# Kernel tuning notes

Hardware: AMD Instinct MI355X
Metric: run time of the kernel (lower is better)

The kernel has to match this reference:

```python
import jax, jax.numpy as jnp
import numpy as np

B, N, DIN, D, HID, C, K = 16, 1024, 768, 512, 128, 20, 64
H = W = 32
EPS = 1e-5  # BatchNorm eps (inference mode with running stats)


def _conv(x, w, pad=0, dil=1):
    return jax.lax.conv_general_dilated(
        x, w, (1, 1), [(pad, pad), (pad, pad)],
        rhs_dilation=(dil, dil),
        dimension_numbers=('NCHW', 'OIHW', 'NCHW'))


def _bn(x, g, b, m, v):
    inv = jax.lax.rsqrt(v + EPS)
    return (x - m[None, :, None, None]) * (g * inv)[None, :, None, None] + b[None, :, None, None]


def _l2norm(x):
    n = jnp.sqrt(jnp.sum(x * x, axis=-1, keepdims=True))
    return x / jnp.maximum(n, 1e-12)  # matches F.normalize(eps=1e-12)


def setup_inputs():
    key = jax.random.key(0)
    ks = jax.random.split(key, 12)

    def conv_w(k, o, i, kh, kw):
        return jax.random.normal(k, (o, i, kh, kw), jnp.float32) / np.sqrt(i * kh * kw)

    def bn_p(k, c):
        k1, k2 = jax.random.split(k)
        return (jnp.ones(c, jnp.float32), jnp.zeros(c, jnp.float32),
                0.1 * jax.random.normal(k1, (c,), jnp.float32),
                jax.random.uniform(k2, (c,), jnp.float32, 0.5, 1.5))

    g0, b0, m0, v0 = bn_p(ks[3], D)
    gr, br, mr, vr = bn_p(ks[4], HID)
    gl, bl, ml, vl = bn_p(ks[5], HID)
    gg, bg, mg, vg = bn_p(ks[6], HID)
    gp, bp, mp, vp = bn_p(ks[7], D)
    return {
        'patch_feats': jax.random.normal(ks[0], (B, N, DIN), jnp.float32),
        'protos': _l2norm(jax.random.normal(ks[1], (C, K, D), jnp.float32)),  # hybrid protos, L2-normed as in __init__
        'w0': conv_w(ks[2], D, DIN, 1, 1), 'g0': g0, 'b0': b0, 'm0': m0, 'v0': v0,
        'wr': conv_w(ks[8], HID, D, 1, 1), 'gr': gr, 'br': br, 'mr': mr, 'vr': vr,
        'wl': conv_w(ks[9], HID, HID, 3, 3), 'gl': gl, 'bl': bl, 'ml': ml, 'vl': vl,
        'wg': conv_w(ks[10], HID, HID, 3, 3), 'gg': gg, 'bg': bg, 'mg': mg, 'vg': vg,
        'wp': conv_w(ks[11], D, 2 * HID, 1, 1), 'gp': gp, 'bp': bp, 'mp': mp, 'vp': vp,
        'wf': conv_w(jax.random.fold_in(key, 99), D, D, 1, 1),
        'bf': jnp.zeros(D, jnp.float32),
        'logit_scale': jnp.float32(10.0),
    }


def reference(patch_feats, protos, w0, g0, b0, m0, v0, wr, gr, br, mr, vr,
              wl, gl, bl, ml, vl, wg, gg, bg, mg, vg, wp, gp, bp, mp, vp,
              wf, bf, logit_scale):
    Bq, Nq, Din = patch_feats.shape
    x = patch_feats.transpose(0, 2, 1).reshape(Bq, Din, H, W)
    # adapter: 1x1 conv -> BN -> ReLU
    x = jax.nn.relu(_bn(_conv(x, w0), g0, b0, m0, v0))
    # ResidualContextBlock
    res = x
    o = jax.nn.relu(_bn(_conv(x, wr), gr, br, mr, vr))
    l = jax.nn.relu(_bn(_conv(o, wl, pad=1), gl, bl, ml, vl))
    g = jax.nn.relu(_bn(_conv(o, wg, pad=2, dil=2), gg, bg, mg, vg))
    o = _bn(_conv(jnp.concatenate([l, g], axis=1), wp), gp, bp, mp, vp)
    x = jax.nn.relu(o + res)
    # final 1x1 conv (with bias)
    x = _conv(x, wf) + bf[None, :, None, None]
    # back to [B, N, D], L2 normalize
    x = x.reshape(Bq, D, Nq).transpose(0, 2, 1)
    x = _l2norm(x)
    # per-class cosine sims + double max reduction (vectorized over classes)
    sims = jnp.einsum('bnd,ckd->bcnk', x, protos)  # [B,C,N,K]
    A = sims.max(axis=-1)                          # [B,C,N] patch->proto max
    act_maps = A.reshape(Bq, C, H, W)
    logits = A.max(axis=-1) * logit_scale          # [B,C]
    return logits, act_maps, x
```

## Files before the change

kernel.cpp:

```cpp
#include <hip/hip_runtime.h>
#include <math.h>

#define BN_EPS 1e-5f

typedef __attribute__((ext_vector_type(8))) short short8v;
typedef __attribute__((ext_vector_type(8))) unsigned short ushort8v;
typedef __attribute__((ext_vector_type(4))) float f32x4;

__device__ __forceinline__ unsigned short f2b(float f) {
    unsigned int u = __float_as_uint(f);
    return (unsigned short)((u + 0x7FFFu + ((u >> 16) & 1u)) >> 16);
}
__device__ __forceinline__ float b2f(unsigned short h) {
    return __uint_as_float(((unsigned int)h) << 16);
}

typedef __attribute__((address_space(1))) const unsigned int gas_uint;
typedef __attribute__((address_space(3))) unsigned int las_uint;
__device__ __forceinline__ void gload16(const void* g, void* l) {
    __builtin_amdgcn_global_load_lds((gas_uint*)g, (las_uint*)l, 16, 0, 0);
}

__global__ __launch_bounds__(256) void f2b_kernel(
    const float* __restrict__ in, unsigned short* __restrict__ out, int n8)
{
    int i = blockIdx.x * 256 + threadIdx.x;
    if (i >= n8) return;
    const float4* p = (const float4*)(in + (size_t)i * 8);
    float4 a = p[0], b = p[1];
    ushort8v r;
    r[0] = f2b(a.x); r[1] = f2b(a.y); r[2] = f2b(a.z); r[3] = f2b(a.w);
    r[4] = f2b(b.x); r[5] = f2b(b.y); r[6] = f2b(b.z); r[7] = f2b(b.w);
    *(ushort8v*)(out + (size_t)i * 8) = r;
}

__global__ __launch_bounds__(256) void f2b_multi(
    const float* __restrict__ w0, const float* __restrict__ wr,
    const float* __restrict__ wp, const float* __restrict__ wf,
    const float* __restrict__ prot,
    unsigned short* __restrict__ w0o, unsigned short* __restrict__ wro,
    unsigned short* __restrict__ wpo, unsigned short* __restrict__ wfo,
    unsigned short* __restrict__ proto)
{
    int i = blockIdx.x * 256 + threadIdx.x;
    const float* src; unsigned short* dst; int off;
    if      (i <  49152) { src = w0;   dst = w0o;   off = i; }
    else if (i <  57344) { src = wr;   dst = wro;   off = i - 49152; }
    else if (i <  73728) { src = wp;   dst = wpo;   off = i - 57344; }
    else if (i < 106496) { src = wf;   dst = wfo;   off = i - 73728; }
    else if (i < 188416) { src = prot; dst = proto; off = i - 106496; }
    else return;
    const float4* p = (const float4*)(src + (size_t)off * 8);
    float4 a = p[0], b = p[1];
    ushort8v r;
    r[0] = f2b(a.x); r[1] = f2b(a.y); r[2] = f2b(a.z); r[3] = f2b(a.w);
    r[4] = f2b(b.x); r[5] = f2b(b.y); r[6] = f2b(b.z); r[7] = f2b(b.w);
    *(ushort8v*)(dst + (size_t)off * 8) = r;
}

__global__ __launch_bounds__(256) void convw_kernel(
    const float* __restrict__ wl, const float* __restrict__ wg,
    unsigned short* __restrict__ out)
{
    int i = blockIdx.x * 256 + threadIdx.x;
    if (i >= 294912) return;
    int br = i >= 147456;
    int j  = i - br * 147456;
    int tap = j >> 14, oc = (j >> 7) & 127, ic = j & 127;
    const float* src = br ? wg : wl;
    out[i] = f2b(src[((oc << 7) + ic) * 9 + tap]);
}

__global__ __launch_bounds__(256) void zero_kernel(unsigned short* __restrict__ p, int n8)
{
    int i = blockIdx.x * 256 + threadIdx.x;
    if (i >= n8) return;
    ushort8v z;
#pragma unroll
    for (int k = 0; k < 8; ++k) z[k] = 0;
    *(ushort8v*)(p + (size_t)i * 8) = z;
}

template <int EPI>
__global__ __launch_bounds__(256) void mfma_gemm(
    const unsigned short* __restrict__ A, int lda,
    const unsigned short* __restrict__ Wt, int ldw,
    void* __restrict__ outp, int ldc, int Kdim,
    const float* __restrict__ bng, const float* __restrict__ bnb,
    const float* __restrict__ bnm, const float* __restrict__ bnv,
    const unsigned short* __restrict__ res, int ldres,
    const float* __restrict__ bias)
{
    __shared__ short8v Asta[512];
    __shared__ short8v Bsta[512];
    const int t  = threadIdx.x;
    const int l  = t & 63, wv = t >> 6;
    const int wm = wv >> 1, wn = wv & 1;
    const int m0 = blockIdx.x << 7, n0 = blockIdx.y << 7;

    const int r0  = t & 127;
    const int kb0 = t >> 7;

    const unsigned short* Ap = A  + (size_t)(m0 + r0) * lda + kb0 * 8;
    const unsigned short* Bp = Wt + (size_t)(n0 + r0) * ldw + kb0 * 8;

    short8v* aD0 = Asta + wv * 64;
    short8v* aD1 = Asta + wv * 64 + 256;
    short8v* bD0 = Bsta + wv * 64;
    short8v* bD1 = Bsta + wv * 64 + 256;

    f32x4 acc[4][4];
#pragma unroll
    for (int mf = 0; mf < 4; ++mf)
#pragma unroll
        for (int nf = 0; nf < 4; ++nf)
#pragma unroll
            for (int j = 0; j < 4; ++j) acc[mf][nf][j] = 0.f;

    const int arow = wm * 64 + (l & 15);
    const int brow = wn * 64 + (l & 15);
    const int kq   = l >> 4;

    for (int k0 = 0; k0 < Kdim; k0 += 32) {
        __syncthreads();
        gload16(Ap + k0,      aD0);
        gload16(Ap + k0 + 16, aD1);
        gload16(Bp + k0,      bD0);
        gload16(Bp + k0 + 16, bD1);
        __syncthreads();
        short8v af[4], bfv[4];
#pragma unroll
        for (int mf = 0; mf < 4; ++mf) af[mf]  = Asta[kq * 128 + arow + mf * 16];
#pragma unroll
        for (int nf = 0; nf < 4; ++nf) bfv[nf] = Bsta[kq * 128 + brow + nf * 16];
#pragma unroll
        for (int mf = 0; mf < 4; ++mf)
#pragma unroll
            for (int nf = 0; nf < 4; ++nf)
                acc[mf][nf] = __builtin_amdgcn_mfma_f32_16x16x32_bf16(
                    af[mf], bfv[nf], acc[mf][nf], 0, 0, 0);
    }

    float s[4], sh[4];
    int cols[4];
#pragma unroll
    for (int nf = 0; nf < 4; ++nf) {
        int col = n0 + wn * 64 + nf * 16 + (l & 15);
        cols[nf] = col;
        if (EPI == 2) { s[nf] = 1.f; sh[nf] = bias[col]; }
        else {
            float sc = bng[col] * rsqrtf(bnv[col] + BN_EPS);
            s[nf]  = sc;
            sh[nf] = bnb[col] - bnm[col] * sc;
        }
    }
#pragma unroll
    for (int mf = 0; mf < 4; ++mf) {
#pragma unroll
        for (int j = 0; j < 4; ++j) {
            int row = m0 + wm * 64 + mf * 16 + kq * 4 + j;
#pragma unroll
            for (int nf = 0; nf < 4; ++nf) {
                float v = acc[mf][nf][j] * s[nf] + sh[nf];
                if (EPI == 1) v += b2f(res[(size_t)row * ldres + cols[nf]]);
                if (EPI != 2) v = fmaxf(v, 0.f);
                if (EPI == 2) {
                    ((float*)outp)[(size_t)row * ldc + cols[nf]] = v;
                } else if (EPI == 3) {
                    int b = row >> 10, h = (row >> 5) & 31, ww = row & 31;
                    size_t pidx = ((size_t)(b * 36 + h + 2) * 36 + (ww + 2)) * 128 + cols[nf];
                    ((unsigned short*)outp)[pidx] = f2b(v);
                } else {
                    ((unsigned short*)outp)[(size_t)row * ldc + cols[nf]] = f2b(v);
                }
            }
        }
    }
}

__global__ __launch_bounds__(256) void conv_mfma(
    const unsigned short* __restrict__ opad,
    const unsigned short* __restrict__ wt_all,
    const float* __restrict__ g1, const float* __restrict__ b1,
    const float* __restrict__ m1, const float* __restrict__ v1,
    const float* __restrict__ g2, const float* __restrict__ b2,
    const float* __restrict__ m2, const float* __restrict__ v2,
    unsigned short* __restrict__ lg)
{
    __shared__ short8v Asta[1024];
    __shared__ short8v Bsta[2048];
    const int t = threadIdx.x;
    const int l = t & 63, wv = t >> 6;
    const int wm = wv >> 1, wn = wv & 1;
    const int m0 = blockIdx.x << 6;
    const int br = blockIdx.y;
    const int dil = 1 + br;
    const unsigned short* wtb = wt_all + (size_t)br * 147456;

    const int r0  = t & 63,  kb0 = t >> 6;
    const int rb  = t & 127, kbb = t >> 7;
    const int m   = m0 + r0;
    const int bb  = m >> 10, h = (m >> 5) & 31, wc = m & 31;
    const ptrdiff_t pbase = ((ptrdiff_t)(bb * 36 + h + 2) * 36 + (wc + 2)) * 128;
    const unsigned short* ApT = opad + pbase + kb0 * 8;
    const unsigned short* BpT = wtb + (size_t)rb * 128 + kbb * 8;

    f32x4 acc[2][4];
#pragma unroll
    for (int mf = 0; mf < 2; ++mf)
#pragma unroll
        for (int nf = 0; nf < 4; ++nf)
#pragma unroll
            for (int j = 0; j < 4; ++j) acc[mf][nf][j] = 0.f;

    const int arow = wm * 32 + (l & 15);
    const int bcol = wn * 64 + (l & 15);
    const int kq   = l >> 4;

    for (int tap = 0; tap < 9; ++tap) {
        const int dh = tap / 3 - 1, dw = tap % 3 - 1;
        const unsigned short* Ap = ApT + (ptrdiff_t)((dh * 36 + dw) * dil) * 128;
        const unsigned short* Bp = BpT + (size_t)tap * 16384;
        __syncthreads();
#pragma unroll
        for (int i = 0; i < 4; ++i)
            gload16(Ap + 32 * i, Asta + wv * 64 + 256 * i);
#pragma unroll
        for (int i = 0; i < 8; ++i)
            gload16(Bp + 16 * i, Bsta + wv * 64 + 256 * i);
        __syncthreads();
#pragma unroll
        for (int kk = 0; kk < 4; ++kk) {
            short8v af[2], bfv[4];
            af[0] = Asta[(kq + 4 * kk) * 64 + arow];
            af[1] = Asta[(kq + 4 * kk) * 64 + arow + 16];
#pragma unroll
            for (int nf = 0; nf < 4; ++nf)
                bfv[nf] = Bsta[(kq + 4 * kk) * 128 + bcol + nf * 16];
#pragma unroll
            for (int mf = 0; mf < 2; ++mf)
#pragma unroll
                for (int nf = 0; nf < 4; ++nf)
                    acc[mf][nf] = __builtin_amdgcn_mfma_f32_16x16x32_bf16(
                        af[mf], bfv[nf], acc[mf][nf], 0, 0, 0);
        }
    }

    const float* gg = br ? g2 : g1;
    const float* gb = br ? b2 : b1;
    const float* gm = br ? m2 : m1;
    const float* gv = br ? v2 : v1;
    float s[4], sh[4];
    int cols[4];
#pragma unroll
    for (int nf = 0; nf < 4; ++nf) {
        int col = bcol + nf * 16;
        cols[nf] = col;
        float sc = gg[col] * rsqrtf(gv[col] + BN_EPS);
        s[nf]  = sc;
        sh[nf] = gb[col] - gm[col] * sc;
    }
#pragma unroll
    for (int mf = 0; mf < 2; ++mf) {
#pragma unroll
        for (int j = 0; j < 4; ++j) {
            int row = m0 + wm * 32 + mf * 16 + kq * 4 + j;
#pragma unroll
            for (int nf = 0; nf < 4; ++nf) {
                float v = fmaxf(acc[mf][nf][j] * s[nf] + sh[nf], 0.f);
                lg[(size_t)row * 256 + br * 128 + cols[nf]] = f2b(v);
            }
        }
    }
}

__global__ __launch_bounds__(256) void l2norm_rows(
    float* __restrict__ x, unsigned short* __restrict__ xn)
{
    const int t    = threadIdx.x;
    const int wv   = t >> 6, lane = t & 63;
    const int row  = (blockIdx.x << 2) + wv;
    float* p = x + (size_t)row * 512 + (lane << 3);
    float4 a = *(float4*)p;
    float4 b = *(float4*)(p + 4);
    float ss = a.x * a.x + a.y * a.y + a.z * a.z + a.w * a.w +
               b.x * b.x + b.y * b.y + b.z * b.z + b.w * b.w;
#pragma unroll
    for (int off = 32; off >= 1; off >>= 1) ss += __shfl_xor(ss, off);
    float sc = 1.f / fmaxf(sqrtf(ss), 1e-12f);
    a.x *= sc; a.y *= sc; a.z *= sc; a.w *= sc;
    b.x *= sc; b.y *= sc; b.z *= sc; b.w *= sc;
    *(float4*)p       = a;
    *(float4*)(p + 4) = b;
    ushort8v r;
    r[0] = f2b(a.x); r[1] = f2b(a.y); r[2] = f2b(a.z); r[3] = f2b(a.w);
    r[4] = f2b(b.x); r[5] = f2b(b.y); r[6] = f2b(b.z); r[7] = f2b(b.w);
    *(ushort8v*)(xn + (size_t)row * 512 + (lane << 3)) = r;
}

__global__ __launch_bounds__(256) void sims_mfma(
    const unsigned short* __restrict__ xn,
    const unsigned short* __restrict__ protos,
    float* __restrict__ act)
{
    __shared__ short8v Asta[512];
    __shared__ short8v Bsta[512];
    const int t = threadIdx.x;
    const int l = t & 63, wv = t >> 6;
    const int wm = wv >> 1, wn = wv & 1;
    const int m0 = blockIdx.x << 7;

    const int r0  = t & 127, kb0 = t >> 7;
    const unsigned short* Ap = xn + (size_t)(m0 + r0) * 512 + kb0 * 8;
    const unsigned short* Bp = protos + ((size_t)blockIdx.y * 128 + r0) * 512 + kb0 * 8;

    short8v* aD0 = Asta + wv * 64;
    short8v* aD1 = Asta + wv * 64 + 256;
    short8v* bD0 = Bsta + wv * 64;
    short8v* bD1 = Bsta + wv * 64 + 256;

    f32x4 acc[4][4];
#pragma unroll
    for (int mf = 0; mf < 4; ++mf)
#pragma unroll
        for (int nf = 0; nf < 4; ++nf)
#pragma unroll
            for (int j = 0; j < 4; ++j) acc[mf][nf][j] = 0.f;

    const int arow = wm * 64 + (l & 15);
    const int brow = wn * 64 + (l & 15);
    const int kq   = l >> 4;

    for (int k0 = 0; k0 < 512; k0 += 32) {
        __syncthreads();
        gload16(Ap + k0,      aD0);
        gload16(Ap + k0 + 16, aD1);
        gload16(Bp + k0,      bD0);
        gload16(Bp + k0 + 16, bD1);
        __syncthreads();
        short8v af[4], bfv[4];
#pragma unroll
        for (int mf = 0; mf < 4; ++mf) af[mf]  = Asta[kq * 128 + arow + mf * 16];
#pragma unroll
        for (int nf = 0; nf < 4; ++nf) bfv[nf] = Bsta[kq * 128 + brow + nf * 16];
#pragma unroll
        for (int mf = 0; mf < 4; ++mf)
#pragma unroll
            for (int nf = 0; nf < 4; ++nf)
                acc[mf][nf] = __builtin_amdgcn_mfma_f32_16x16x32_bf16(
                    af[mf], bfv[nf], acc[mf][nf], 0, 0, 0);
    }

    const int c = (blockIdx.y << 1) + wn;
#pragma unroll
    for (int mf = 0; mf < 4; ++mf) {
        float vj[4];
#pragma unroll
        for (int j = 0; j < 4; ++j) {
            float v = fmaxf(fmaxf(acc[mf][0][j], acc[mf][1][j]),
                            fmaxf(acc[mf][2][j], acc[mf][3][j]));
            v = fmaxf(v, __shfl_xor(v, 1));
            v = fmaxf(v, __shfl_xor(v, 2));
            v = fmaxf(v, __shfl_xor(v, 4));
            v = fmaxf(v, __shfl_xor(v, 8));
            vj[j] = v;
        }
        if ((l & 15) == 0) {
            int rowb = m0 + wm * 64 + mf * 16 + kq * 4;
#pragma unroll
            for (int j = 0; j < 4; ++j) {
                int row = rowb + j;
                int bb = row >> 10, n = row & 1023;
                act[(((size_t)(bb * 20 + c)) << 10) + n] = vj[j];
            }
        }
    }
}

__global__ __launch_bounds__(256) void logits_max(
    const float* __restrict__ act, const float* __restrict__ lsc,
    float* __restrict__ logits)
{
    const int bc = blockIdx.x;
    const int t  = threadIdx.x;
    float4 v = *(const float4*)(act + ((size_t)bc << 10) + (t << 2));
    float mx = fmaxf(fmaxf(v.x, v.y), fmaxf(v.z, v.w));
#pragma unroll
    for (int off = 32; off >= 1; off >>= 1) mx = fmaxf(mx, __shfl_xor(mx, off));
    __shared__ float wmred[4];
    if ((t & 63) == 0) wmred[t >> 6] = mx;
    __syncthreads();
    if (t == 0) {
        float m2 = fmaxf(fmaxf(wmred[0], wmred[1]), fmaxf(wmred[2], wmred[3]));
        logits[bc] = m2 * lsc[0];
    }
}

extern "C" void kernel_launch(void* const* d_in, const int* in_sizes, int n_in,
                              void* d_out, int out_size, void* d_ws, size_t ws_size,
                              hipStream_t stream)
{
    const float* pf   = (const float*)d_in[0];
    const float* prot = (const float*)d_in[1];
    const float* w0   = (const float*)d_in[2];
    const float* g0   = (const float*)d_in[3];
    const float* b0   = (const float*)d_in[4];
    const float* m0v  = (const float*)d_in[5];
    const float* v0   = (const float*)d_in[6];
    const float* wr   = (const float*)d_in[7];
    const float* gr   = (const float*)d_in[8];
    const float* br   = (const float*)d_in[9];
    const float* mr   = (const float*)d_in[10];
    const float* vr   = (const float*)d_in[11];
    const float* wl   = (const float*)d_in[12];
    const float* gl   = (const float*)d_in[13];
    const float* bl   = (const float*)d_in[14];
    const float* ml   = (const float*)d_in[15];
    const float* vl   = (const float*)d_in[16];
    const float* wg   = (const float*)d_in[17];
    const float* gG   = (const float*)d_in[18];
    const float* bG   = (const float*)d_in[19];
    const float* mG   = (const float*)d_in[20];
    const float* vG   = (const float*)d_in[21];
    const float* wp   = (const float*)d_in[22];
    const float* gp   = (const float*)d_in[23];
    const float* bp   = (const float*)d_in[24];
    const float* mp   = (const float*)d_in[25];
    const float* vp   = (const float*)d_in[26];
    const float* wf   = (const float*)d_in[27];
    const float* bf_  = (const float*)d_in[28];
    const float* lsc  = (const float*)d_in[29];

    char* ws = (char*)d_ws;
    unsigned short* pf_bf    = (unsigned short*)(ws);
    unsigned short* w0_bf    = (unsigned short*)(ws + 25165824);
    unsigned short* wr_bf    = (unsigned short*)(ws + 25952256);
    unsigned short* wt_bf    = (unsigned short*)(ws + 26083328);
    unsigned short* wp_bf    = (unsigned short*)(ws + 26673152);
    unsigned short* wf_bf    = (unsigned short*)(ws + 26935296);
    unsigned short* prot_bf  = (unsigned short*)(ws + 27459584);
    unsigned short* x1_bf    = (unsigned short*)(ws + 28770304);
    unsigned short* opad     = (unsigned short*)(ws + 45547520);
    unsigned short* lg_bf    = (unsigned short*)(ws + 50855936);
    unsigned short* x2_bf    = (unsigned short*)(ws + 59244544);
    unsigned short* xn_bf    = (unsigned short*)(ws + 76021760);

    float* out    = (float*)d_out;
    float* logits = out;
    float* act    = out + 320;
    float* xo     = out + 328000;

    f2b_kernel<<<6144, 256, 0, stream>>>(pf, pf_bf, 1572864);
    f2b_multi<<<736, 256, 0, stream>>>(w0, wr, wp, wf, prot,
                                       w0_bf, wr_bf, wp_bf, wf_bf, prot_bf);
    convw_kernel<<<1152, 256, 0, stream>>>(wl, wg, wt_bf);
    zero_kernel<<<1296, 256, 0, stream>>>(opad, 331776);

    mfma_gemm<0><<<dim3(128, 4), 256, 0, stream>>>(
        pf_bf, 768, w0_bf, 768, x1_bf, 512, 768,
        g0, b0, m0v, v0, nullptr, 0, nullptr);

    mfma_gemm<3><<<dim3(128, 1), 256, 0, stream>>>(
        x1_bf, 512, wr_bf, 512, opad, 0, 512,
        gr, br, mr, vr, nullptr, 0, nullptr);

    conv_mfma<<<dim3(256, 2), 256, 0, stream>>>(
        opad, wt_bf, gl, bl, ml, vl, gG, bG, mG, vG, lg_bf);

    mfma_gemm<1><<<dim3(128, 4), 256, 0, stream>>>(
        lg_bf, 256, wp_bf, 256, x2_bf, 512, 256,
        gp, bp, mp, vp, x1_bf, 512, nullptr);

    mfma_gemm<2><<<dim3(128, 4), 256, 0, stream>>>(
        x2_bf, 512, wf_bf, 512, xo, 512, 512,
        nullptr, nullptr, nullptr, nullptr, nullptr, 0, bf_);

    l2norm_rows<<<4096, 256, 0, stream>>>(xo, xn_bf);

    sims_mfma<<<dim3(128, 10), 256, 0, stream>>>(xn_bf, prot_bf, act);

    logits_max<<<320, 256, 0, stream>>>(act, lsc, logits);
}
```

Baseline: 202.0 us.

## Double-buffer LDS staging in GEMM, conv and sims kernels to overlap loads

Converts the three MFMA kernels from a single-buffered load/sync/compute loop to a double-buffered scheme. The next K-slice is prefetched into the alternate LDS buffer while the current slice's MFMAs run, and one barrier per iteration replaces two. The conv kernel now splits each tap into two 64-wide K halves so its per-stage LDS footprint fits the two buffers. Launch bounds with min 3 blocks per CU are also added, which may constrain register allocation.

After: 198.0 us. -2.0%, faster.

```diff
diff --git a/kernel.cpp b/kernel.cpp
--- a/kernel.cpp
+++ b/kernel.cpp
@@ -82,7 +82,7 @@
 }
 
 template <int EPI>
-__global__ __launch_bounds__(256) void mfma_gemm(
+__global__ __launch_bounds__(256, 3) void mfma_gemm(
     const unsigned short* __restrict__ A, int lda,
     const unsigned short* __restrict__ Wt, int ldw,
     void* __restrict__ outp, int ldc, int Kdim,
@@ -91,8 +91,8 @@
     const unsigned short* __restrict__ res, int ldres,
     const float* __restrict__ bias)
 {
-    __shared__ short8v Asta[512];
-    __shared__ short8v Bsta[512];
+    __shared__ short8v Asta[2][512];
+    __shared__ short8v Bsta[2][512];
     const int t  = threadIdx.x;
     const int l  = t & 63, wv = t >> 6;
     const int wm = wv >> 1, wn = wv & 1;
@@ -104,11 +104,6 @@
     const unsigned short* Ap = A  + (size_t)(m0 + r0) * lda + kb0 * 8;
     const unsigned short* Bp = Wt + (size_t)(n0 + r0) * ldw + kb0 * 8;
 
-    short8v* aD0 = Asta + wv * 64;
-    short8v* aD1 = Asta + wv * 64 + 256;
-    short8v* bD0 = Bsta + wv * 64;
-    short8v* bD1 = Bsta + wv * 64 + 256;
-
     f32x4 acc[4][4];
 #pragma unroll
     for (int mf = 0; mf < 4; ++mf)
@@ -121,25 +116,36 @@
     const int brow = wn * 64 + (l & 15);
     const int kq   = l >> 4;
 
-    for (int k0 = 0; k0 < Kdim; k0 += 32) {
-        __syncthreads();
-        gload16(Ap + k0,      aD0);
-        gload16(Ap + k0 + 16, aD1);
-        gload16(Bp + k0,      bD0);
-        gload16(Bp + k0 + 16, bD1);
-        __syncthreads();
+    const int nK = Kdim >> 5;
+
+#define STAGE_G(buf, k0)                                     \
+    do {                                                     \
+        gload16(Ap + (k0),      &Asta[buf][wv * 64]);        \
+        gload16(Ap + (k0) + 16, &Asta[buf][wv * 64 + 256]);  \
+        gload16(Bp + (k0),      &Bsta[buf][wv * 64]);        \
+        gload16(Bp + (k0) + 16, &Bsta[buf][wv * 64 + 256]);  \
+    } while (0)
+
+    STAGE_G(0, 0);
+    __syncthreads();
+    int cur = 0;
+    for (int ks = 0; ks < nK; ++ks) {
         short8v af[4], bfv[4];
 #pragma unroll
-        for (int mf = 0; mf < 4; ++mf) af[mf]  = Asta[kq * 128 + arow + mf * 16];
-#pragma unroll
-        for (int nf = 0; nf < 4; ++nf) bfv[nf] = Bsta[kq * 128 + brow + nf * 16];
+        for (int mf = 0; mf < 4; ++mf) af[mf]  = Asta[cur][kq * 128 + arow + mf * 16];
+#pragma unroll
+        for (int nf = 0; nf < 4; ++nf) bfv[nf] = Bsta[cur][kq * 128 + brow + nf * 16];
+        if (ks + 1 < nK) STAGE_G(cur ^ 1, (ks + 1) << 5);
 #pragma unroll
         for (int mf = 0; mf < 4; ++mf)
 #pragma unroll
             for (int nf = 0; nf < 4; ++nf)
                 acc[mf][nf] = __builtin_amdgcn_mfma_f32_16x16x32_bf16(
                     af[mf], bfv[nf], acc[mf][nf], 0, 0, 0);
-    }
+        __syncthreads();
+        cur ^= 1;
+    }
+#undef STAGE_G
 
     float s[4], sh[4];
     int cols[4];
@@ -178,7 +184,7 @@
     }
 }
 
-__global__ __launch_bounds__(256) void conv_mfma(
+__global__ __launch_bounds__(256, 3) void conv_mfma(
     const unsigned short* __restrict__ opad,
     const unsigned short* __restrict__ wt_all,
     const float* __restrict__ g1, const float* __restrict__ b1,
@@ -187,8 +193,8 @@
     const float* __restrict__ m2, const float* __restrict__ v2,
     unsigned short* __restrict__ lg)
 {
-    __shared__ short8v Asta[1024];
-    __shared__ short8v Bsta[2048];
+    __shared__ short8v Asta[2][512];
+    __shared__ short8v Bsta[2][1024];
     const int t = threadIdx.x;
     const int l = t & 63, wv = t >> 6;
     const int wm = wv >> 1, wn = wv & 1;
@@ -197,13 +203,12 @@
     const int dil = 1 + br;
     const unsigned short* wtb = wt_all + (size_t)br * 147456;
 
-    const int r0  = t & 63,  kb0 = t >> 6;
-    const int rb  = t & 127, kbb = t >> 7;
-    const int m   = m0 + r0;
-    const int bb  = m >> 10, h = (m >> 5) & 31, wc = m & 31;
+    const int r0 = t & 63;
+    const int m  = m0 + r0;
+    const int bb = m >> 10, h = (m >> 5) & 31, wc = m & 31;
     const ptrdiff_t pbase = ((ptrdiff_t)(bb * 36 + h + 2) * 36 + (wc + 2)) * 128;
-    const unsigned short* ApT = opad + pbase + kb0 * 8;
-    const unsigned short* BpT = wtb + (size_t)rb * 128 + kbb * 8;
+    const unsigned short* ApT = opad + pbase + (t >> 6) * 8;
+    const unsigned short* BpT = wtb + (size_t)(t & 127) * 128 + (t >> 7) * 8;
 
     f32x4 acc[2][4];
 #pragma unroll
@@ -217,47 +222,60 @@
     const int bcol = wn * 64 + (l & 15);
     const int kq   = l >> 4;
 
-    for (int tap = 0; tap < 9; ++tap) {
-        const int dh = tap / 3 - 1, dw = tap % 3 - 1;
-        const unsigned short* Ap = ApT + (ptrdiff_t)((dh * 36 + dw) * dil) * 128;
-        const unsigned short* Bp = BpT + (size_t)tap * 16384;
-        __syncthreads();
-#pragma unroll
-        for (int i = 0; i < 4; ++i)
-            gload16(Ap + 32 * i, Asta + wv * 64 + 256 * i);
-#pragma unroll
-        for (int i = 0; i < 8; ++i)
-            gload16(Bp + 16 * i, Bsta + wv * 64 + 256 * i);
-        __syncthreads();
-#pragma unroll
-        for (int kk = 0; kk < 4; ++kk) {
-            short8v af[2], bfv[4];
-            af[0] = Asta[(kq + 4 * kk) * 64 + arow];
-            af[1] = Asta[(kq + 4 * kk) * 64 + arow + 16];
+#define STAGE_C(buf, s)                                                        \
+    do {                                                                       \
+        int tap_ = (s) >> 1, hh_ = ((s) & 1) * 64;                             \
+        int dh_ = tap_ / 3 - 1, dw_ = tap_ % 3 - 1;                            \
+        const unsigned short* Ap_ = ApT + (ptrdiff_t)((dh_ * 36 + dw_) * dil) * 128 + hh_; \
+        const unsigned short* Bp_ = BpT + (size_t)tap_ * 16384 + hh_;          \
+        gload16(Ap_,      &Asta[buf][wv * 64]);                                \
+        gload16(Ap_ + 32, &Asta[buf][wv * 64 + 256]);                          \
+        gload16(Bp_,      &Bsta[buf][wv * 64]);                                \
+        gload16(Bp_ + 16, &Bsta[buf][wv * 64 + 256]);                          \
+        gload16(Bp_ + 32, &Bsta[buf][wv * 64 + 512]);                          \
+        gload16(Bp_ + 48, &Bsta[buf][wv * 64 + 768]);                          \
+    } while (0)
+
+    STAGE_C(0, 0);
+    __syncthreads();
+    int cur = 0;
+    for (int s = 0; s < 18; ++s) {
+        short8v af[2][2], bfv[2][4];
+#pragma unroll
+        for (int kk = 0; kk < 2; ++kk) {
+            int kb = kk * 4 + kq;
+            af[kk][0] = Asta[cur][kb * 64 + arow];
+            af[kk][1] = Asta[cur][kb * 64 + arow + 16];
 #pragma unroll
             for (int nf = 0; nf < 4; ++nf)
-                bfv[nf] = Bsta[(kq + 4 * kk) * 128 + bcol + nf * 16];
+                bfv[kk][nf] = Bsta[cur][kb * 128 + bcol + nf * 16];
+        }
+        if (s + 1 < 18) STAGE_C(cur ^ 1, s + 1);
+#pragma unroll
+        for (int kk = 0; kk < 2; ++kk)
 #pragma unroll
             for (int mf = 0; mf < 2; ++mf)
 #pragma unroll
                 for (int nf = 0; nf < 4; ++nf)
                     acc[mf][nf] = __builtin_amdgcn_mfma_f32_16x16x32_bf16(
-                        af[mf], bfv[nf], acc[mf][nf], 0, 0, 0);
-        }
-    }
+                        af[kk][mf], bfv[kk][nf], acc[mf][nf], 0, 0, 0);
+        __syncthreads();
+        cur ^= 1;
+    }
+#undef STAGE_C
 
     const float* gg = br ? g2 : g1;
     const float* gb = br ? b2 : b1;
     const float* gm = br ? m2 : m1;
     const float* gv = br ? v2 : v1;
-    float s[4], sh[4];
+    float s4[4], sh[4];
     int cols[4];
 #pragma unroll
     for (int nf = 0; nf < 4; ++nf) {
         int col = bcol + nf * 16;
         cols[nf] = col;
         float sc = gg[col] * rsqrtf(gv[col] + BN_EPS);
-        s[nf]  = sc;
+        s4[nf] = sc;
         sh[nf] = gb[col] - gm[col] * sc;
     }
 #pragma unroll
@@ -267,7 +285,7 @@
             int row = m0 + wm * 32 + mf * 16 + kq * 4 + j;
 #pragma unroll
             for (int nf = 0; nf < 4; ++nf) {
-                float v = fmaxf(acc[mf][nf][j] * s[nf] + sh[nf], 0.f);
+                float v = fmaxf(acc[mf][nf][j] * s4[nf] + sh[nf], 0.f);
                 lg[(size_t)row * 256 + br * 128 + cols[nf]] = f2b(v);
             }
         }
@@ -298,13 +316,13 @@
     *(ushort8v*)(xn + (size_t)row * 512 + (lane << 3)) = r;
 }
 
-__global__ __launch_bounds__(256) void sims_mfma(
+__global__ __launch_bounds__(256, 3) void sims_mfma(
     const unsigned short* __restrict__ xn,
     const unsigned short* __restrict__ protos,
     float* __restrict__ act)
 {
-    __shared__ short8v Asta[512];
-    __shared__ short8v Bsta[512];
+    __shared__ short8v Asta[2][512];
+    __shared__ short8v Bsta[2][512];
     const int t = threadIdx.x;
     const int l = t & 63, wv = t >> 6;
     const int wm = wv >> 1, wn = wv & 1;
@@ -314,11 +332,6 @@
     const unsigned short* Ap = xn + (size_t)(m0 + r0) * 512 + kb0 * 8;
     const unsigned short* Bp = protos + ((size_t)blockIdx.y * 128 + r0) * 512 + kb0 * 8;
 
-    short8v* aD0 = Asta + wv * 64;
-    short8v* aD1 = Asta + wv * 64 + 256;
-    short8v* bD0 = Bsta + wv * 64;
-    short8v* bD1 = Bsta + wv * 64 + 256;
-
     f32x4 acc[4][4];
 #pragma unroll
     for (int mf = 0; mf < 4; ++mf)
@@ -331,25 +344,34 @@
     const int brow = wn * 64 + (l & 15);
     const int kq   = l >> 4;
 
-    for (int k0 = 0; k0 < 512; k0 += 32) {
-        __syncthreads();
-        gload16(Ap + k0,      aD0);
-        gload16(Ap + k0 + 16, aD1);
-        gload16(Bp + k0,      bD0);
-        gload16(Bp + k0 + 16, bD1);
-        __syncthreads();
+#define STAGE_S(buf, k0)                                     \
+    do {                                                     \
+        gload16(Ap + (k0),      &Asta[buf][wv * 64]);        \
+        gload16(Ap + (k0) + 16, &Asta[buf][wv * 64 + 256]);  \
+        gload16(Bp + (k0),      &Bsta[buf][wv * 64]);        \
+        gload16(Bp + (k0) + 16, &Bsta[buf][wv * 64 + 256]);  \
+    } while (0)
+
+    STAGE_S(0, 0);
+    __syncthreads();
+    int cur = 0;
+    for (int ks = 0; ks < 16; ++ks) {
         short8v af[4], bfv[4];
 #pragma unroll
-        for (int mf = 0; mf < 4; ++mf) af[mf]  = Asta[kq * 128 + arow + mf * 16];
-#pragma unroll
-        for (int nf = 0; nf < 4; ++nf) bfv[nf] = Bsta[kq * 128 + brow + nf * 16];
+        for (int mf = 0; mf < 4; ++mf) af[mf]  = Asta[cur][kq * 128 + arow + mf * 16];
+#pragma unroll
+        for (int nf = 0; nf < 4; ++nf) bfv[nf] = Bsta[cur][kq * 128 + brow + nf * 16];
+        if (ks + 1 < 16) STAGE_S(cur ^ 1, (ks + 1) << 5);
 #pragma unroll
         for (int mf = 0; mf < 4; ++mf)
 #pragma unroll
             for (int nf = 0; nf < 4; ++nf)
                 acc[mf][nf] = __builtin_amdgcn_mfma_f32_16x16x32_bf16(
                     af[mf], bfv[nf], acc[mf][nf], 0, 0, 0);
-    }
+        __syncthreads();
+        cur ^= 1;
+    }
+#undef STAGE_S
 
     const int c = (blockIdx.y << 1) + wn;
 #pragma unroll
```
